# Kernel tuning notes

Hardware: AMD Instinct MI355X
Metric: run time of the kernel (lower is better)

The kernel has to match this reference:

```python
import jax, jax.numpy as jnp
import numpy as np

B, N, L, D, H = 2, 2048, 2048, 1024, 16
HD = D // H  # 64


def setup_inputs() -> dict:
    key = jax.random.key(0)
    ks = jax.random.split(key, 12)
    s = 0.02
    return {
        "x_q": jax.random.normal(ks[0], (B, N, D), jnp.float32),
        "x_kv": jax.random.normal(ks[1], (B, L, D), jnp.float32),
        "pad_mask": jax.random.randint(ks[2], (B, L), 0, 2) > 0,
        "wq": jax.random.normal(ks[3], (D, D), jnp.float32) * s,
        "bq": jnp.zeros((D,), jnp.float32),
        "wk": jax.random.normal(ks[4], (D, D), jnp.float32) * s,
        "bk": jnp.zeros((D,), jnp.float32),
        "wv": jax.random.normal(ks[5], (D, D), jnp.float32) * s,
        "bv": jnp.zeros((D,), jnp.float32),
        "wo": jax.random.normal(ks[6], (D, D), jnp.float32) * s,
        "bo": jnp.zeros((D,), jnp.float32),
    }


def reference(x_q, x_kv, pad_mask, wq, bq, wk, bk, wv, bv, wo, bo):
    scale = HD ** -0.5
    # projections: (B, S, D) -> (B, H, S, HD)
    def split_heads(x):
        return x.reshape(x.shape[0], x.shape[1], H, HD).transpose(0, 2, 1, 3)
    q = split_heads(x_q @ wq + bq) * scale
    k = split_heads(x_kv @ wk + bk)
    v = split_heads(x_kv @ wv + bv)
    attn = jnp.einsum('bhic,bhjc->bhij', q, k)  # (B, H, N, L)
    neg = -jnp.finfo(attn.dtype).max
    attn = jnp.where(pad_mask[:, None, None, :], neg, attn)
    attn = jax.nn.softmax(attn, axis=-1)
    o = jnp.einsum('bhij,bhjc->bhic', attn, v)  # (B, H, N, HD)
    o = o.transpose(0, 2, 1, 3).reshape(B, N, D)
    return o @ wo + bo
```

## Files before the change

### kernel.cpp

```cpp
#include <hip/hip_runtime.h>
#include <hip/hip_bf16.h>
#include <math.h>

typedef __bf16 bf16;
typedef __attribute__((ext_vector_type(8))) __bf16 bf16x8;
typedef __attribute__((ext_vector_type(4))) __bf16 bf16x4;
typedef __attribute__((ext_vector_type(4))) float floatx4;
typedef __attribute__((ext_vector_type(16))) float floatx16;

#define BB 2
#define NN 2048
#define LL 2048
#define DD 1024
#define HH 16
#define HDD 64

#define QSCALE (0.125f * 1.44269504f)
#define PCLAMP 21.66f
#define MBIAS  (-100000.0f)

__device__ __forceinline__ void async16(const bf16* g, bf16* l) {
  __builtin_amdgcn_global_load_lds((const __attribute__((address_space(1))) void*)(g),
                                   (__attribute__((address_space(3))) void*)(l), 16, 0, 0);
}

__device__ __forceinline__ unsigned cvtpk(float a, float b) {
  unsigned r;
  asm("v_cvt_pk_bf16_f32 %0, %1, %2" : "=v"(r) : "v"(a), "v"(b));
  return r;
}

__device__ __forceinline__ void plswap(unsigned &x, unsigned &y) {
  auto r = __builtin_amdgcn_permlane32_swap(x, y, false, false);
  x = (unsigned)r[0];
  y = (unsigned)r[1];
}

__device__ __forceinline__ bf16x8 mk_frag(unsigned w0, unsigned w1, unsigned w2, unsigned w3) {
  union { unsigned u[4]; bf16x8 b; } f;
  f.u[0] = w0; f.u[1] = w1; f.u[2] = w2; f.u[3] = w3;
  return f.b;
}

__global__ __launch_bounds__(256) void prep_kernel(
    const float* __restrict__ xq, const float* __restrict__ xkv,
    bf16* __restrict__ Xqb, bf16* __restrict__ Xkvb, int nconv, int elemsEach,
    const float* __restrict__ W0, const float* __restrict__ W1,
    const float* __restrict__ W2, const float* __restrict__ W3,
    bf16* __restrict__ T0, bf16* __restrict__ T1,
    bf16* __restrict__ T2, bf16* __restrict__ T3,
    const unsigned* __restrict__ mask, float* __restrict__ biasF)
{
  __shared__ bf16 Tb[64][72];
  const int bid = blockIdx.x;
  const int t = threadIdx.x;

  if (bid < nconv) {
    const int half = nconv >> 1;
    const float* s = (bid < half) ? xq : xkv;
    bf16* d = (bid < half) ? Xqb : Xkvb;
    int gid = (bid < half) ? bid : bid - half;
    int idx = (gid * 256 + t) * 8;
    if (idx >= elemsEach) return;
    floatx4 a = *(const floatx4*)&s[idx];
    floatx4 b = *(const floatx4*)&s[idx + 4];
    bf16x8 o;
#pragma unroll
    for (int e = 0; e < 4; e++) { o[e] = (bf16)a[e]; o[4 + e] = (bf16)b[e]; }
    *(bf16x8*)&d[idx] = o;
    return;
  }
  if (bid < nconv + 1024) {
    const int wb = bid - nconv;
    const int which = wb >> 8;
    const float* W = which == 0 ? W0 : which == 1 ? W1 : which == 2 ? W2 : W3;
    bf16*       T = which == 0 ? T0 : which == 1 ? T1 : which == 2 ? T2 : T3;
    const int tile = wb & 255;
    const int k0 = (tile >> 4) * 64, n0 = (tile & 15) * 64;
    const int r = t >> 2;
    const int c = (t & 3) * 16;
    const float* Wr = W + (size_t)(k0 + r) * 1024 + n0 + c;
    floatx4 f0 = *(const floatx4*)(Wr + 0);
    floatx4 f1 = *(const floatx4*)(Wr + 4);
    floatx4 f2 = *(const floatx4*)(Wr + 8);
    floatx4 f3 = *(const floatx4*)(Wr + 12);
#pragma unroll
    for (int e = 0; e < 4; e++) {
      Tb[c + e][r]      = (bf16)f0[e];
      Tb[c + 4 + e][r]  = (bf16)f1[e];
      Tb[c + 8 + e][r]  = (bf16)f2[e];
      Tb[c + 12 + e][r] = (bf16)f3[e];
    }
    __syncthreads();
    bf16* Tr = T + (size_t)(n0 + r) * 1024 + k0 + c;
    *(bf16x8*)&Tr[0] = *(const bf16x8*)&Tb[r][c];
    *(bf16x8*)&Tr[8] = *(const bf16x8*)&Tb[r][c + 8];
    return;
  }
  __shared__ int hasBig, hasFloat;
  if (t == 0) { hasBig = 0; hasFloat = 0; }
  __syncthreads();
  int big = 0, flt = 0;
  for (int idx = t; idx < 1024; idx += 256) {
    unsigned v = mask[idx];
    if (v == 0x3F800000u) flt = 1;
    else if (v > 1u) big = 1;
  }
  if (big) atomicOr(&hasBig, 1);
  if (flt) atomicOr(&hasFloat, 1);
  __syncthreads();
  const int mode = hasFloat ? 2 : (hasBig ? 1 : 0);
  for (int k = t * 16; k < t * 16 + 16; k++) {
    bool m;
    if (mode == 0)      m = ((const int*)mask)[k] != 0;
    else if (mode == 1) m = ((const unsigned char*)mask)[k] != 0;
    else                m = ((const float*)mask)[k] != 0.0f;
    biasF[k] = m ? MBIAS : 0.0f;
  }
}

template <typename TC>
__device__ __forceinline__ void gemm_body32(
    int bx, const bf16* __restrict__ A, const bf16* __restrict__ Wt,
    const float* __restrict__ bias, TC* __restrict__ C, float scale, int transv)
{
  __shared__ bf16 As[3][128 * 32];
  __shared__ bf16 Bs[3][128 * 32];

  const int tm = bx >> 3, tn = bx & 7;
  const int m0 = tm * 128, n0 = tn * 128;
  const int t = threadIdx.x;
  const int w = t >> 6, l = t & 63;
  const int col = l & 31, half = l >> 5;
  const int wm = (w >> 1) * 64, wn = (w & 1) * 64;
  const int sr  = t >> 2;
  const int scl = (t & 3) * 8;
  const int scs = (((t & 3) ^ ((t >> 3) & 3)) * 8);
  const int csw = (col >> 1) & 3;

  floatx16 acc[2][2];
#pragma unroll
  for (int mi = 0; mi < 2; mi++)
#pragma unroll
    for (int ni = 0; ni < 2; ni++)
#pragma unroll
      for (int e = 0; e < 16; e++) acc[mi][ni][e] = 0.0f;

  auto STAGE = [&](int k0, int s) {
    async16(&A[(size_t)(m0 + sr) * 1024 + k0 + scs],       &As[s][sr * 32 + scl]);
    async16(&A[(size_t)(m0 + 64 + sr) * 1024 + k0 + scs],  &As[s][(64 + sr) * 32 + scl]);
    async16(&Wt[(size_t)(n0 + sr) * 1024 + k0 + scs],      &Bs[s][sr * 32 + scl]);
    async16(&Wt[(size_t)(n0 + 64 + sr) * 1024 + k0 + scs], &Bs[s][(64 + sr) * 32 + scl]);
  };

  STAGE(0, 0);
  const int NK = 1024 / 32;
  for (int k = 0; k < NK; k++) {
    if (k + 1 < NK) {
      STAGE((k + 1) * 32, (k + 1) % 3);
      asm volatile("s_waitcnt vmcnt(4)" ::: "memory");
    } else {
      asm volatile("s_waitcnt vmcnt(0)" ::: "memory");
    }
    __builtin_amdgcn_s_barrier();
    __builtin_amdgcn_sched_barrier(0);
    const bf16* as = &As[k % 3][0];
    const bf16* bs = &Bs[k % 3][0];
#pragma unroll
    for (int kk = 0; kk < 2; kk++) {
      const int ch = ((kk * 2 + half) ^ csw) * 8;
      bf16x8 af[2], bfr[2];
#pragma unroll
      for (int mi = 0; mi < 2; mi++)
        af[mi] = *(const bf16x8*)&as[(wm + mi * 32 + col) * 32 + ch];
#pragma unroll
      for (int ni = 0; ni < 2; ni++)
        bfr[ni] = *(const bf16x8*)&bs[(wn + ni * 32 + col) * 32 + ch];
#pragma unroll
      for (int mi = 0; mi < 2; mi++)
#pragma unroll
        for (int ni = 0; ni < 2; ni++)
          acc[mi][ni] = __builtin_amdgcn_mfma_f32_32x32x16_bf16(af[mi], bfr[ni], acc[mi][ni], 0, 0, 0);
    }
  }
#pragma unroll
  for (int ni = 0; ni < 2; ni++) {
    int colg = n0 + wn + ni * 32 + col;
    float bv = bias[colg];
#pragma unroll
    for (int mi = 0; mi < 2; mi++) {
      int rbase = m0 + wm + mi * 32 + half * 4;
      if (transv) {
#pragma unroll
        for (int g = 0; g < 4; g++) {
          int key0 = rbase + g * 8;
          int bb = key0 >> 11, key = key0 & 2047;
          bf16x4 v4;
#pragma unroll
          for (int r = 0; r < 4; r++) v4[r] = (bf16)(acc[mi][ni][g * 4 + r] + bv);
          *(bf16x4*)&((bf16*)C)[(size_t)bb * (DD * (size_t)LL) + (size_t)colg * LL + key] = v4;
        }
      } else {
#pragma unroll
        for (int g = 0; g < 4; g++)
#pragma unroll
          for (int r = 0; r < 4; r++)
            C[(size_t)(rbase + g * 8 + r) * 1024 + colg] = (TC)((acc[mi][ni][g * 4 + r] + bv) * scale);
      }
    }
  }
}

__global__ __launch_bounds__(256) void qkv_gemm32(
    const bf16* __restrict__ Xq, const bf16* __restrict__ Xkv,
    const bf16* __restrict__ Wtq, const bf16* __restrict__ Wtk, const bf16* __restrict__ Wtv,
    const float* __restrict__ bq, const float* __restrict__ bk, const float* __restrict__ bv,
    bf16* __restrict__ Qp, bf16* __restrict__ Kp, bf16* __restrict__ VtG, int shift)
{
  const int bid = blockIdx.x;
  const int which = bid >> shift;
  const int bx0 = bid & ((1 << shift) - 1);
  const int q = (1 << shift) >> 3;
  const int bx = (bx0 & 7) * q + (bx0 >> 3);
  if (which == 0)      gemm_body32<bf16>(bx, Xq,  Wtq, bq, Qp,  QSCALE, 0);
  else if (which == 1) gemm_body32<bf16>(bx, Xkv, Wtk, bk, Kp,  1.0f,   0);
  else                 gemm_body32<bf16>(bx, Xkv, Wtv, bv, VtG, 1.0f,   1);
}

__global__ __launch_bounds__(256) void out_gemm(
    const bf16* __restrict__ A, const bf16* __restrict__ Wt,
    const float* __restrict__ bias, float* __restrict__ C)
{
  __shared__ bf16 As[3][128 * 32];
  __shared__ bf16 Bs[3][64 * 32];

  const int bid = blockIdx.x;
  const int qs = gridDim.x >> 3;
  const int bx = (bid & 7) * qs + (bid >> 3);
  const int tm = bx >> 4, tn = bx & 15;
  const int m0 = tm * 128, n0 = tn * 64;
  const int t = threadIdx.x;
  const int w = t >> 6, l = t & 63;
  const int q = l >> 4, i = l & 15;
  const int wm = (w >> 1) * 64, wn = (w & 1) * 32;
  const int sr  = t >> 2;
  const int scl = (t & 3) * 8;
  const int scs = (((t & 3) ^ ((t >> 3) & 3)) * 8);
  const int isw = (i >> 1) & 3;

  const floatx4 zero = {0.f, 0.f, 0.f, 0.f};
  floatx4 acc[4][2];
#pragma unroll
  for (int mi = 0; mi < 4; mi++)
#pragma unroll
    for (int ni = 0; ni < 2; ni++) acc[mi][ni] = zero;

  auto STAGE = [&](int k0, int s) {
    async16(&A[(size_t)(m0 + sr) * 1024 + k0 + scs],       &As[s][sr * 32 + scl]);
    async16(&A[(size_t)(m0 + 64 + sr) * 1024 + k0 + scs],  &As[s][(64 + sr) * 32 + scl]);
    async16(&Wt[(size_t)(n0 + sr) * 1024 + k0 + scs],      &Bs[s][sr * 32 + scl]);
  };

  STAGE(0, 0);
  const int NK = 1024 / 32;
  for (int k = 0; k < NK; k++) {
    if (k + 1 < NK) {
      STAGE((k + 1) * 32, (k + 1) % 3);
      asm volatile("s_waitcnt vmcnt(3)" ::: "memory");
    } else {
      asm volatile("s_waitcnt vmcnt(0)" ::: "memory");
    }
    __builtin_amdgcn_s_barrier();
    __builtin_amdgcn_sched_barrier(0);
    const bf16* as = &As[k % 3][0];
    const bf16* bs = &Bs[k % 3][0];
    const int ch = (q ^ isw) * 8;
    bf16x8 af[4], bfr[2];
#pragma unroll
    for (int mi = 0; mi < 4; mi++)
      af[mi] = *(const bf16x8*)&as[(wm + mi * 16 + i) * 32 + ch];
#pragma unroll
    for (int ni = 0; ni < 2; ni++)
      bfr[ni] = *(const bf16x8*)&bs[(wn + ni * 16 + i) * 32 + ch];
#pragma unroll
    for (int mi = 0; mi < 4; mi++)
#pragma unroll
      for (int ni = 0; ni < 2; ni++)
        acc[mi][ni] = __builtin_amdgcn_mfma_f32_16x16x32_bf16(af[mi], bfr[ni], acc[mi][ni], 0, 0, 0);
  }
#pragma unroll
  for (int ni = 0; ni < 2; ni++) {
    int colg = n0 + wn + ni * 16 + i;
    float bv = bias[colg];
#pragma unroll
    for (int mi = 0; mi < 4; mi++) {
      int row = m0 + wm + mi * 16 + q * 4;
#pragma unroll
      for (int r = 0; r < 4; r++)
        C[(size_t)(row + r) * 1024 + colg] = acc[mi][ni][r] + bv;
    }
  }
}

__global__ __launch_bounds__(512, 4) void attn_kernel(
    const bf16* __restrict__ Q, const bf16* __restrict__ K,
    const bf16* __restrict__ Vt, const float* __restrict__ biasF,
    bf16* __restrict__ O, int hbits)
{
  __shared__ __align__(16) char smem[73728];
  bf16* KVl = (bf16*)smem;
  float* biasLds = (float*)(smem + 65536);

  const int bid = blockIdx.x;
  const int qt = bid >> hbits;
  const int hb = bid & ((1 << hbits) - 1);
  const int h  = (hbits == 5) ? (hb >> 1) : hb;
  const int b  = (hbits == 5) ? (hb & 1) : 0;
  const int t = threadIdx.x;
  const int w = t >> 6, lane = t & 63;
  const int kg = w >> 2;
  const int wi = w & 3;
  const int col = lane & 31;
  const int hi  = lane >> 5;
  const int lsw = lane & 7;

  const bf16* Qb = Q  + (size_t)b * (NN * DD) + h * HDD;
  const bf16* Kb = K  + (size_t)b * (LL * DD) + h * HDD;
  const bf16* Vb = Vt + (size_t)b * (DD * (size_t)LL) + (size_t)(h * HDD) * LL;
  const float* biasFb = biasF + b * LL;

  const int qrow = qt * 128 + wi * 32;

  bf16x8 qfrag[4];
#pragma unroll
  for (int dc = 0; dc < 4; dc++)
    qfrag[dc] = *(const bf16x8*)&Qb[(size_t)(qrow + col) * DD + dc * 16 + hi * 8];

  floatx16 oacc[2];
#pragma unroll
  for (int db = 0; db < 2; db++)
#pragma unroll
    for (int e = 0; e < 16; e++) oacc[db][e] = 0.0f;
  float psum = 0.0f;

  *(floatx4*)&biasLds[t * 4] = *(const floatx4*)&biasFb[t * 4];

  const int tl  = t & 255;
  const int sr  = tl >> 3;
  const int scl = (tl & 7) * 8;
  const int scs = ((tl & 7) ^ (sr & 7)) * 8;

  auto STAGE = [&](int tile, int slot) {
    const int k0 = tile * 64;
    bf16* Kd = KVl + (kg * 2 + slot) * 4096;
    bf16* Vd = KVl + 16384 + (kg * 2 + slot) * 4096;
    async16(&Kb[(size_t)(k0 + sr) * DD + scs],      Kd + sr * 64 + scl);
    async16(&Kb[(size_t)(k0 + sr + 32) * DD + scs], Kd + (sr + 32) * 64 + scl);
    async16(&Vb[(size_t)sr * LL + k0 + scs],        Vd + sr * 64 + scl);
    async16(&Vb[(size_t)(sr + 32) * LL + k0 + scs], Vd + (sr + 32) * 64 + scl);
  };

  STAGE(kg * 16, 0);

  bf16x8 pfp[4];
  floatx16 sacc[2];

  const int NTg = 16;
  for (int i = 0; i < NTg; i++) {
    const int T = kg * 16 + i;
    const int slot = i & 1;
    __syncthreads();
    if (i + 1 < NTg) STAGE(T + 1, (i + 1) & 1);

    const bf16* Kc = KVl + (kg * 2 + slot) * 4096;
    const bf16* Vc = KVl + 16384 + (kg * 2 + slot) * 4096;

    const int kn = T * 64;
#pragma unroll
    for (int kb = 0; kb < 2; kb++)
#pragma unroll
      for (int gg = 0; gg < 4; gg++) {
        floatx4 pbv = *(const floatx4*)&biasLds[kn + kb * 32 + gg * 8 + hi * 4];
#pragma unroll
        for (int rr = 0; rr < 4; rr++) sacc[kb][gg * 4 + rr] = pbv[rr];
      }
    __builtin_amdgcn_s_setprio(1);
#pragma unroll
    for (int kb = 0; kb < 2; kb++)
#pragma unroll
      for (int dc = 0; dc < 4; dc++) {
        bf16x8 kf = *(const bf16x8*)&Kc[(kb * 32 + col) * 64 + ((dc * 2 + hi) ^ lsw) * 8];
        sacc[kb] = __builtin_amdgcn_mfma_f32_32x32x16_bf16(kf, qfrag[dc], sacc[kb], 0, 0, 0);
      }
    __builtin_amdgcn_s_setprio(0);

#pragma unroll
    for (int kb = 0; kb < 2; kb++)
#pragma unroll
      for (int hh = 0; hh < 2; hh++) {
        float pv[8];
#pragma unroll
        for (int e = 0; e < 8; e++) {
          float p = __builtin_amdgcn_exp2f(fminf(sacc[kb][hh * 8 + e], PCLAMP));
          psum += p;
          pv[e] = p;
        }
        unsigned a0 = cvtpk(pv[0], pv[1]);
        unsigned a1 = cvtpk(pv[2], pv[3]);
        unsigned b0 = cvtpk(pv[4], pv[5]);
        unsigned b1 = cvtpk(pv[6], pv[7]);
        plswap(a0, b0);
        plswap(a1, b1);
        pfp[kb * 2 + hh] = mk_frag(a0, a1, b0, b1);
      }

    __builtin_amdgcn_s_setprio(1);
#pragma unroll
    for (int db = 0; db < 2; db++)
#pragma unroll
      for (int kc = 0; kc < 4; kc++) {
        bf16x8 vf = *(const bf16x8*)&Vc[(db * 32 + col) * 64 + ((kc * 2 + hi) ^ lsw) * 8];
        oacc[db] = __builtin_amdgcn_mfma_f32_32x32x16_bf16(vf, pfp[kc], oacc[db], 0, 0, 0);
      }
    __builtin_amdgcn_s_setprio(0);
  }

  __syncthreads();
  float* sOacc = (float*)smem;
  float* sPsum = (float*)(smem + 4 * 64 * 33 * 4);
  if (kg == 1) {
    const int base = (wi * 64 + lane) * 33;
#pragma unroll
    for (int db = 0; db < 2; db++)
#pragma unroll
      for (int e = 0; e < 16; e++)
        sOacc[base + db * 16 + e] = oacc[db][e];
    sPsum[wi * 64 + lane] = psum;
  }
  __syncthreads();
  if (kg == 0) {
    const int base = (wi * 64 + lane) * 33;
#pragma unroll
    for (int db = 0; db < 2; db++)
#pragma unroll
      for (int e = 0; e < 16; e++)
        oacc[db][e] += sOacc[base + db * 16 + e];
    psum += sPsum[wi * 64 + lane];
    psum += __shfl_xor(psum, 32, 64);
    float inv = 1.0f / fmaxf(psum, 1e-30f);

    bf16* Ob = O + (size_t)b * (NN * DD) + h * HDD;
#pragma unroll
    for (int db = 0; db < 2; db++)
#pragma unroll
      for (int gg = 0; gg < 4; gg++) {
        bf16x4 v4;
#pragma unroll
        for (int rr = 0; rr < 4; rr++) v4[rr] = (bf16)(oacc[db][gg * 4 + rr] * inv);
        *(bf16x4*)&Ob[(size_t)(qrow + col) * DD + db * 32 + gg * 8 + hi * 4] = v4;
      }
  }
}

extern "C" void kernel_launch(void* const* d_in, const int* in_sizes, int n_in,
                              void* d_out, int out_size, void* d_ws, size_t ws_size,
                              hipStream_t stream)
{
  const float* x_q  = (const float*)d_in[0];
  const float* x_kv = (const float*)d_in[1];
  const void*  pad  = d_in[2];
  const float* wq = (const float*)d_in[3];
  const float* bq = (const float*)d_in[4];
  const float* wk = (const float*)d_in[5];
  const float* bk = (const float*)d_in[6];
  const float* wv = (const float*)d_in[7];
  const float* bv = (const float*)d_in[8];
  const float* wo = (const float*)d_in[9];
  const float* bo = (const float*)d_in[10];
  float* out = (float*)d_out;

  char* ws = (char*)d_ws;
  const size_t MB = (size_t)1 << 20;
  const size_t fullElems = (size_t)BB * NN * DD;
  const size_t batchElems = (size_t)NN * DD;

  if (ws_size >= 49 * MB) {
    bf16* Xqb   = (bf16*)(ws);
    bf16* Xkvb  = (bf16*)(ws + 8 * MB);
    bf16* Wtq   = (bf16*)(ws + 16 * MB);
    bf16* Wtk   = (bf16*)(ws + 18 * MB);
    bf16* Wtv   = (bf16*)(ws + 20 * MB);
    bf16* Wto   = (bf16*)(ws + 22 * MB);
    bf16* Qp    = (bf16*)(ws + 24 * MB);
    bf16* Kp    = (bf16*)(ws + 32 * MB);
    bf16* VtG   = (bf16*)(ws + 40 * MB);
    float* biasF = (float*)(ws + 48 * MB);
    bf16* Op    = Xqb;

    prep_kernel<<<5121, 256, 0, stream>>>(x_q, x_kv, Xqb, Xkvb, 4096, (int)fullElems,
                                          wq, wk, wv, wo, Wtq, Wtk, Wtv, Wto,
                                          (const unsigned*)pad, biasF);
    qkv_gemm32<<<768, 256, 0, stream>>>(Xqb, Xkvb, Wtq, Wtk, Wtv, bq, bk, bv, Qp, Kp, VtG, 8);
    attn_kernel<<<512, 512, 0, stream>>>(Qp, Kp, VtG, biasF, Op, 5);
    out_gemm<<<512, 256, 0, stream>>>(Op, Wto, bo, out);
  } else {
    bf16* Wtq   = (bf16*)(ws);
    bf16* Wtk   = (bf16*)(ws + 2 * MB);
    bf16* Wtv   = (bf16*)(ws + 4 * MB);
    bf16* Wto   = (bf16*)(ws + 6 * MB);
    bf16* Xqb   = (bf16*)(ws + 8 * MB);
    bf16* Xkvb  = (bf16*)(ws + 12 * MB);
    bf16* Qp    = (bf16*)(ws + 16 * MB);
    bf16* Kp    = (bf16*)(ws + 20 * MB);
    bf16* VtG   = (bf16*)(ws + 24 * MB);
    float* biasF = (float*)(ws + 28 * MB);
    bf16* Op    = Xqb;

    for (int b = 0; b < BB; b++) {
      if (b == 0)
        prep_kernel<<<3073, 256, 0, stream>>>(x_q, x_kv, Xqb, Xkvb, 2048, (int)batchElems,
                                              wq, wk, wv, wo, Wtq, Wtk, Wtv, Wto,
                                              (const unsigned*)pad, biasF);
      else
        prep_kernel<<<2048, 256, 0, stream>>>(x_q + b * batchElems, x_kv + b * batchElems,
                                              Xqb, Xkvb, 2048, (int)batchElems,
                                              wq, wk, wv, wo, Wtq, Wtk, Wtv, Wto,
                                              (const unsigned*)pad, biasF);
      qkv_gemm32<<<384, 256, 0, stream>>>(Xqb, Xkvb, Wtq, Wtk, Wtv, bq, bk, bv, Qp, Kp, VtG, 7);
      attn_kernel<<<256, 512, 0, stream>>>(Qp, Kp, VtG, biasF + b * LL, Op, 4);
      out_gemm<<<256, 256, 0, stream>>>(Op, Wto, bo, out + b * batchElems);
    }
  }
}
```

Baseline: 209.3 us.

## Split attention across four KV groups with 64-row query tiles and smaller LDS

The attention kernel now gives each block 64 query rows instead of 128 and splits the KV sequence across four wave groups of 512 keys each, in place of two groups of 1024. Each group stages 32-key tiles in a single LDS buffer instead of double-buffered 64-key tiles. Shared memory drops from 72 KB to 40 KB, the launch-bounds occupancy hint rises from 4 to 8 and the grid doubles, all to raise occupancy and parallelism. In exchange, double buffering is gone (each iteration waits at a barrier and then issues the next load), barrier count per key roughly doubles, and the final cross-group reduction becomes a two-level tree with extra syncs.

```diff
diff --git a/kernel.cpp b/kernel.cpp
--- a/kernel.cpp
+++ b/kernel.cpp
@@ -302,14 +302,14 @@
   }
 }
 
-__global__ __launch_bounds__(512, 4) void attn_kernel(
+__global__ __launch_bounds__(512, 8) void attn_kernel(
     const bf16* __restrict__ Q, const bf16* __restrict__ K,
     const bf16* __restrict__ Vt, const float* __restrict__ biasF,
     bf16* __restrict__ O, int hbits)
 {
-  __shared__ __align__(16) char smem[73728];
+  __shared__ __align__(16) char smem[40960];
   bf16* KVl = (bf16*)smem;
-  float* biasLds = (float*)(smem + 65536);
+  float* biasLds = (float*)(smem + 32768);
 
   const int bid = blockIdx.x;
   const int qt = bid >> hbits;
@@ -318,18 +318,19 @@
   const int b  = (hbits == 5) ? (hb & 1) : 0;
   const int t = threadIdx.x;
   const int w = t >> 6, lane = t & 63;
-  const int kg = w >> 2;
-  const int wi = w & 3;
+  const int kg = w >> 1;
+  const int wi = w & 1;
   const int col = lane & 31;
   const int hi  = lane >> 5;
   const int lsw = lane & 7;
+  const int vsw = lane & 3;
 
   const bf16* Qb = Q  + (size_t)b * (NN * DD) + h * HDD;
   const bf16* Kb = K  + (size_t)b * (LL * DD) + h * HDD;
   const bf16* Vb = Vt + (size_t)b * (DD * (size_t)LL) + (size_t)(h * HDD) * LL;
   const float* biasFb = biasF + b * LL;
 
-  const int qrow = qt * 128 + wi * 32;
+  const int qrow = qt * 64 + wi * 32;
 
   bf16x8 qfrag[4];
 #pragma unroll
@@ -345,107 +346,121 @@
 
   *(floatx4*)&biasLds[t * 4] = *(const floatx4*)&biasFb[t * 4];
 
-  const int tl  = t & 255;
-  const int sr  = tl >> 3;
-  const int scl = (tl & 7) * 8;
-  const int scs = ((tl & 7) ^ (sr & 7)) * 8;
-
-  auto STAGE = [&](int tile, int slot) {
-    const int k0 = tile * 64;
-    bf16* Kd = KVl + (kg * 2 + slot) * 4096;
-    bf16* Vd = KVl + 16384 + (kg * 2 + slot) * 4096;
-    async16(&Kb[(size_t)(k0 + sr) * DD + scs],      Kd + sr * 64 + scl);
-    async16(&Kb[(size_t)(k0 + sr + 32) * DD + scs], Kd + (sr + 32) * 64 + scl);
-    async16(&Vb[(size_t)sr * LL + k0 + scs],        Vd + sr * 64 + scl);
-    async16(&Vb[(size_t)(sr + 32) * LL + k0 + scs], Vd + (sr + 32) * 64 + scl);
+  const int tl  = t & 127;
+  const int ksr = tl >> 3;
+  const int kcl = (tl & 7) * 8;
+  const int kcs = ((tl & 7) ^ (ksr & 7)) * 8;
+  const int vr  = tl >> 2;
+  const int vcl = (tl & 3) * 8;
+  const int vcs = ((tl & 3) ^ (vr & 3)) * 8;
+
+  bf16* Kd = KVl + kg * 2048;
+  bf16* Vd = KVl + 8192 + kg * 2048;
+
+  auto STAGE = [&](int i) {
+    const int k0 = kg * 512 + i * 32;
+    async16(&Kb[(size_t)(k0 + ksr) * DD + kcs],      Kd + ksr * 64 + kcl);
+    async16(&Kb[(size_t)(k0 + ksr + 16) * DD + kcs], Kd + (ksr + 16) * 64 + kcl);
+    async16(&Vb[(size_t)vr * LL + k0 + vcs],         Vd + vr * 32 + vcl);
+    async16(&Vb[(size_t)(vr + 32) * LL + k0 + vcs],  Vd + (vr + 32) * 32 + vcl);
   };
 
-  STAGE(kg * 16, 0);
-
-  bf16x8 pfp[4];
-  floatx16 sacc[2];
+  STAGE(0);
+
+  bf16x8 pfp[2];
+  floatx16 sacc;
 
   const int NTg = 16;
   for (int i = 0; i < NTg; i++) {
-    const int T = kg * 16 + i;
-    const int slot = i & 1;
     __syncthreads();
-    if (i + 1 < NTg) STAGE(T + 1, (i + 1) & 1);
-
-    const bf16* Kc = KVl + (kg * 2 + slot) * 4096;
-    const bf16* Vc = KVl + 16384 + (kg * 2 + slot) * 4096;
-
-    const int kn = T * 64;
-#pragma unroll
-    for (int kb = 0; kb < 2; kb++)
-#pragma unroll
-      for (int gg = 0; gg < 4; gg++) {
-        floatx4 pbv = *(const floatx4*)&biasLds[kn + kb * 32 + gg * 8 + hi * 4];
-#pragma unroll
-        for (int rr = 0; rr < 4; rr++) sacc[kb][gg * 4 + rr] = pbv[rr];
+
+    const int kn = kg * 512 + i * 32;
+
+#pragma unroll
+    for (int gg = 0; gg < 4; gg++) {
+      floatx4 pbv = *(const floatx4*)&biasLds[kn + gg * 8 + hi * 4];
+#pragma unroll
+      for (int rr = 0; rr < 4; rr++) sacc[gg * 4 + rr] = pbv[rr];
+    }
+    __builtin_amdgcn_s_setprio(1);
+#pragma unroll
+    for (int dc = 0; dc < 4; dc++) {
+      bf16x8 kf = *(const bf16x8*)&Kd[col * 64 + ((dc * 2 + hi) ^ lsw) * 8];
+      sacc = __builtin_amdgcn_mfma_f32_32x32x16_bf16(kf, qfrag[dc], sacc, 0, 0, 0);
+    }
+    __builtin_amdgcn_s_setprio(0);
+
+#pragma unroll
+    for (int hh = 0; hh < 2; hh++) {
+      float pv[8];
+#pragma unroll
+      for (int e = 0; e < 8; e++) {
+        float p = __builtin_amdgcn_exp2f(fminf(sacc[hh * 8 + e], PCLAMP));
+        psum += p;
+        pv[e] = p;
       }
+      unsigned a0 = cvtpk(pv[0], pv[1]);
+      unsigned a1 = cvtpk(pv[2], pv[3]);
+      unsigned b0 = cvtpk(pv[4], pv[5]);
+      unsigned b1 = cvtpk(pv[6], pv[7]);
+      plswap(a0, b0);
+      plswap(a1, b1);
+      pfp[hh] = mk_frag(a0, a1, b0, b1);
+    }
+
     __builtin_amdgcn_s_setprio(1);
 #pragma unroll
-    for (int kb = 0; kb < 2; kb++)
-#pragma unroll
-      for (int dc = 0; dc < 4; dc++) {
-        bf16x8 kf = *(const bf16x8*)&Kc[(kb * 32 + col) * 64 + ((dc * 2 + hi) ^ lsw) * 8];
-        sacc[kb] = __builtin_amdgcn_mfma_f32_32x32x16_bf16(kf, qfrag[dc], sacc[kb], 0, 0, 0);
-      }
-    __builtin_amdgcn_s_setprio(0);
-
-#pragma unroll
-    for (int kb = 0; kb < 2; kb++)
-#pragma unroll
-      for (int hh = 0; hh < 2; hh++) {
-        float pv[8];
-#pragma unroll
-        for (int e = 0; e < 8; e++) {
-          float p = __builtin_amdgcn_exp2f(fminf(sacc[kb][hh * 8 + e], PCLAMP));
-          psum += p;
-          pv[e] = p;
-        }
-        unsigned a0 = cvtpk(pv[0], pv[1]);
-        unsigned a1 = cvtpk(pv[2], pv[3]);
-        unsigned b0 = cvtpk(pv[4], pv[5]);
-        unsigned b1 = cvtpk(pv[6], pv[7]);
-        plswap(a0, b0);
-        plswap(a1, b1);
-        pfp[kb * 2 + hh] = mk_frag(a0, a1, b0, b1);
-      }
-
-    __builtin_amdgcn_s_setprio(1);
-#pragma unroll
     for (int db = 0; db < 2; db++)
 #pragma unroll
-      for (int kc = 0; kc < 4; kc++) {
-        bf16x8 vf = *(const bf16x8*)&Vc[(db * 32 + col) * 64 + ((kc * 2 + hi) ^ lsw) * 8];
+      for (int kc = 0; kc < 2; kc++) {
+        bf16x8 vf = *(const bf16x8*)&Vd[(db * 32 + col) * 32 + ((kc * 2 + hi) ^ vsw) * 8];
         oacc[db] = __builtin_amdgcn_mfma_f32_32x32x16_bf16(vf, pfp[kc], oacc[db], 0, 0, 0);
       }
     __builtin_amdgcn_s_setprio(0);
+
+    __syncthreads();
+    if (i + 1 < NTg) STAGE(i + 1);
   }
 
   __syncthreads();
-  float* sOacc = (float*)smem;
-  float* sPsum = (float*)(smem + 4 * 64 * 33 * 4);
-  if (kg == 1) {
-    const int base = (wi * 64 + lane) * 33;
+  float* sO = (float*)smem;
+  float* sP = (float*)smem + 2 * 128 * 33;
+  const int gtl = wi * 64 + lane;
+
+  if (kg & 1) {
+    float* d = sO + (kg >> 1) * (128 * 33) + gtl * 33;
 #pragma unroll
     for (int db = 0; db < 2; db++)
 #pragma unroll
-      for (int e = 0; e < 16; e++)
-        sOacc[base + db * 16 + e] = oacc[db][e];
-    sPsum[wi * 64 + lane] = psum;
+      for (int e = 0; e < 16; e++) d[db * 16 + e] = oacc[db][e];
+    sP[(kg >> 1) * 128 + gtl] = psum;
+  }
+  __syncthreads();
+  if (!(kg & 1)) {
+    const float* d = sO + (kg >> 1) * (128 * 33) + gtl * 33;
+#pragma unroll
+    for (int db = 0; db < 2; db++)
+#pragma unroll
+      for (int e = 0; e < 16; e++) oacc[db][e] += d[db * 16 + e];
+    psum += sP[(kg >> 1) * 128 + gtl];
+  }
+  __syncthreads();
+  if (kg == 2) {
+    float* d = sO + gtl * 33;
+#pragma unroll
+    for (int db = 0; db < 2; db++)
+#pragma unroll
+      for (int e = 0; e < 16; e++) d[db * 16 + e] = oacc[db][e];
+    sP[gtl] = psum;
   }
   __syncthreads();
   if (kg == 0) {
-    const int base = (wi * 64 + lane) * 33;
+    const float* d = sO + gtl * 33;
 #pragma unroll
     for (int db = 0; db < 2; db++)
 #pragma unroll
-      for (int e = 0; e < 16; e++)
-        oacc[db][e] += sOacc[base + db * 16 + e];
-    psum += sPsum[wi * 64 + lane];
+      for (int e = 0; e < 16; e++) oacc[db][e] += d[db * 16 + e];
+    psum += sP[gtl];
     psum += __shfl_xor(psum, 32, 64);
     float inv = 1.0f / fmaxf(psum, 1e-30f);
 
@@ -501,7 +516,7 @@
                                           wq, wk, wv, wo, Wtq, Wtk, Wtv, Wto,
                                           (const unsigned*)pad, biasF);
     qkv_gemm32<<<768, 256, 0, stream>>>(Xqb, Xkvb, Wtq, Wtk, Wtv, bq, bk, bv, Qp, Kp, VtG, 8);
-    attn_kernel<<<512, 512, 0, stream>>>(Qp, Kp, VtG, biasF, Op, 5);
+    attn_kernel<<<1024, 512, 0, stream>>>(Qp, Kp, VtG, biasF, Op, 5);
     out_gemm<<<512, 256, 0, stream>>>(Op, Wto, bo, out);
   } else {
     bf16* Wtq   = (bf16*)(ws);
@@ -527,7 +542,7 @@
                                               wq, wk, wv, wo, Wtq, Wtk, Wtv, Wto,
                                               (const unsigned*)pad, biasF);
       qkv_gemm32<<<384, 256, 0, stream>>>(Xqb, Xkvb, Wtq, Wtk, Wtv, bq, bk, bv, Qp, Kp, VtG, 7);
-      attn_kernel<<<256, 512, 0, stream>>>(Qp, Kp, VtG, biasF + b * LL, Op, 4);
+      attn_kernel<<<512, 512, 0, stream>>>(Qp, Kp, VtG, biasF + b * LL, Op, 4);
       out_gemm<<<256, 256, 0, stream>>>(Op, Wto, bo, out + b * batchElems);
     }
   }
```

New measurement: 304.8 us. 1.46x slower.
